# Optimization experiments

Hardware: AMD Instinct MI355X
Metric: run time of the kernel (lower is better)

Reference implementation:

```python
import jax, jax.numpy as jnp
import numpy as np

HID = 1024   # hidden_dim
H = 16       # num_head
D = 64       # head_dim
W = 64       # window_size (one-sided attention radius)


def setup_inputs() -> dict:
    key = jax.random.key(0)
    ks = jax.random.split(key, 10)
    B, S = 2, 4096
    s = 0.02
    X = jax.random.normal(ks[0], (B, S, HID), jnp.float32)
    mask = jnp.ones((B, S), jnp.float32)
    Wq = jax.random.normal(ks[1], (HID, H * D), jnp.float32) * s
    bq = jnp.zeros((H * D,), jnp.float32)
    Wk = jax.random.normal(ks[2], (HID, H * D), jnp.float32) * s
    bk = jnp.zeros((H * D,), jnp.float32)
    Wv = jax.random.normal(ks[3], (HID, H * D), jnp.float32) * s
    bv = jnp.zeros((H * D,), jnp.float32)
    Wo = jax.random.normal(ks[4], (H * D, HID), jnp.float32) * s
    bo = jnp.zeros((HID,), jnp.float32)
    return dict(X=X, mask=mask, Wq=Wq, bq=bq, Wk=Wk, bk=bk, Wv=Wv, bv=bv, Wo=Wo, bo=bo)


def _chunk3(T, nC):
    # T: [B,H,S,D] -> [B,H,nC,3W,D]: for chunk c, keys of chunks c-1, c, c+1 (zero-padded at ends)
    B, Hh, S, Dd = T.shape
    Tp = jnp.pad(T, ((0, 0), (0, 0), (W, W), (0, 0))).reshape(B, Hh, nC + 2, W, Dd)
    return jnp.concatenate([Tp[:, :, :-2], Tp[:, :, 1:-1], Tp[:, :, 2:]], axis=3)


def reference(X, mask, Wq, bq, Wk, bk, Wv, bv, Wo, bo):
    B, S0, _ = X.shape
    pad = W - S0 % W  # matches torch: always >= 1 (full window if divisible)
    Xp = jnp.pad(X, ((0, 0), (0, pad), (0, 0)))
    mp = jnp.pad(mask, ((0, 0), (0, pad)))  # padded keys masked out
    S = S0 + pad
    nC = S // W

    def proj(Wm, b):
        return (Xp @ Wm + b).reshape(B, S, H, D).transpose(0, 2, 1, 3)  # [B,H,S,D]

    Q, K, V = proj(Wq, bq), proj(Wk, bk), proj(Wv, bv)
    Qc = Q.reshape(B, H, nC, W, D)
    K3 = _chunk3(K, nC)
    V3 = _chunk3(V, nC)

    # banded scores: query i attends keys j with |i - j| <= W
    scores = jnp.einsum('bhcqd,bhckd->bhcqk', Qc, K3) / jnp.asarray(np.sqrt(D), jnp.float32)
    qi = jnp.arange(W)[:, None]
    kj = jnp.arange(3 * W)[None, :]
    band = (kj >= qi) & (kj <= qi + 2 * W)  # [W, 3W]
    m3 = jnp.pad(mp, ((0, 0), (W, W))).reshape(B, nC + 2, W)
    m3 = jnp.concatenate([m3[:, :-2], m3[:, 1:-1], m3[:, 2:]], axis=2)  # [B,nC,3W]
    valid = band[None, None, None, :, :] & (m3[:, None, :, None, :] > 0)
    scores = jnp.where(valid, scores, -1e9)
    A = jax.nn.softmax(scores, axis=-1)
    ctx = jnp.einsum('bhcqk,bhckd->bhcqd', A, V3).reshape(B, H, S, D)
    out = ctx.transpose(0, 2, 1, 3).reshape(B, S, H * D) @ Wo + bo
    return out[:, :S0]
```

## Files before the change

kernel.cpp:

```cpp
#include <hip/hip_runtime.h>

typedef unsigned short u16;
typedef unsigned int u32;
typedef __bf16 bf16x8 __attribute__((ext_vector_type(8)));
typedef u16 u16x8 __attribute__((ext_vector_type(8)));
typedef float floatx4 __attribute__((ext_vector_type(4)));

#define MFMA16(a, b, c) __builtin_amdgcn_mfma_f32_16x16x32_bf16((a), (b), (c), 0, 0, 0)

#define B_ 2
#define S0 4096
#define NH 16
#define HD 64
#define HID 1024
#define VSTR 216

__device__ __forceinline__ float bf2f(u16 u) {
  union { u32 i; float f; } x; x.i = ((u32)u) << 16; return x.f;
}
__device__ __forceinline__ u16 f2bf(float f) {
  union { float f; u32 i; } x; x.f = f;
  u32 r = x.i + 0x7FFFu + ((x.i >> 16) & 1u);
  return (u16)(r >> 16);
}

__device__ __forceinline__ void glds16(const u16* g, u16* l) {
  __builtin_amdgcn_global_load_lds(
      (const __attribute__((address_space(1))) u32*)g,
      (__attribute__((address_space(3))) u32*)l, 16, 0, 0);
}

__global__ __launch_bounds__(256) void prep(
    const float* __restrict__ X, const float* __restrict__ mask,
    const float* __restrict__ Wq, const float* __restrict__ bq,
    const float* __restrict__ Wk, const float* __restrict__ bk,
    const float* __restrict__ Wv, const float* __restrict__ bv,
    const float* __restrict__ Wo, const float* __restrict__ bo,
    u16* __restrict__ cX, u16* __restrict__ cmask, u16* __restrict__ cb,
    u16* __restrict__ WqkvT, u16* __restrict__ WoT) {
  __shared__ u16 tile[64][66];
  int bid = blockIdx.x;
  if (bid < 4096) {
    int i = (bid * 256 + threadIdx.x) * 8;
    u16x8 v;
#pragma unroll
    for (int j = 0; j < 8; j++) v[j] = f2bf(X[i + j]);
    *(u16x8*)(cX + i) = v;
  } else if (bid < 4144) {
    int tid = (bid - 4096) * 256 + threadIdx.x;
    if (tid < B_ * S0) {
      cmask[tid] = f2bf(mask[tid]);
    } else {
      int j = tid - B_ * S0;
      int seg = j >> 10, idx = j & 1023;
      const float* src = (seg == 0) ? bq : (seg == 1) ? bk : (seg == 2) ? bv : bo;
      cb[seg * 1024 + idx] = f2bf(src[idx]);
    }
  } else {
    int idx = bid - 4144;
    int mat = idx >> 8;
    const float* src = (mat == 0) ? Wq : (mat == 1) ? Wk : (mat == 2) ? Wv : Wo;
    u16* dst = (mat < 3) ? (WqkvT + (size_t)mat * HID * HID) : WoT;
    int t0 = ((idx >> 4) & 15) * 64;
    int c0 = (idx & 15) * 64;
    int tx = threadIdx.x & 63, ty = threadIdx.x >> 6;
#pragma unroll
    for (int i = 0; i < 16; i++) {
      int r = i * 4 + ty;
      tile[r][tx] = f2bf(src[(size_t)(t0 + r) * HID + c0 + tx]);
    }
    __syncthreads();
#pragma unroll
    for (int i = 0; i < 16; i++) {
      int r = i * 4 + ty;
      dst[(size_t)(c0 + r) * HID + t0 + tx] = tile[tx][r];
    }
  }
}

template <int BN, int MODE>
__global__ __launch_bounds__(256) void gemm_bf16_tn(
    const u16* __restrict__ A, const u16* __restrict__ Bt,
    const u16* __restrict__ cb, void* __restrict__ outp, int K) {
  constexpr int NT = BN / 32;
  __shared__ alignas(16) u16 sA[128 * 64];
  __shared__ alignas(16) u16 sB[BN * 64];
  int t = threadIdx.x;
  int wave = t >> 6, lane = t & 63;
  int wm = wave >> 1, wn = wave & 1;
  int quad = lane >> 4, l16 = lane & 15;
  int tile_m = blockIdx.x * 128;
  int tile_n = blockIdx.y * BN;

  floatx4 acc[4][NT] = {};

  int row_l = lane >> 3;
  int col_l = ((lane & 7) ^ row_l) * 8;
  const u16* Ag = A + (size_t)(tile_m + wave * 8 + row_l) * K + col_l;
  const u16* Bg = Bt + (size_t)(tile_n + wave * 8 + row_l) * K + col_l;
  u16* lA = sA + wave * 8 * 64;
  u16* lB = sB + wave * 8 * 64;

  for (int k0 = 0; k0 < K; k0 += 64) {
    __syncthreads();
#pragma unroll
    for (int r = 0; r < 4; r++)
      glds16(Ag + (size_t)(r * 32) * K + k0, lA + r * 2048);
#pragma unroll
    for (int r = 0; r < BN / 32; r++)
      glds16(Bg + (size_t)(r * 32) * K + k0, lB + r * 2048);
    __syncthreads();

#pragma unroll
    for (int ks = 0; ks < 2; ks++) {
      bf16x8 af[4], bfr[NT];
#pragma unroll
      for (int mt = 0; mt < 4; mt++) {
        int row = wm * 64 + mt * 16 + l16;
        int p = (ks * 4 + quad) ^ (row & 7);
        af[mt] = *(const bf16x8*)(sA + row * 64 + p * 8);
      }
#pragma unroll
      for (int nt = 0; nt < NT; nt++) {
        int row = wn * (BN / 2) + nt * 16 + l16;
        int p = (ks * 4 + quad) ^ (row & 7);
        bfr[nt] = *(const bf16x8*)(sB + row * 64 + p * 8);
      }
#pragma unroll
      for (int mt = 0; mt < 4; mt++)
#pragma unroll
        for (int nt = 0; nt < NT; nt++)
          acc[mt][nt] = MFMA16(af[mt], bfr[nt], acc[mt][nt]);
    }
  }

  if (MODE == 0) {
    u16* op = (u16*)outp;
#pragma unroll
    for (int mt = 0; mt < 4; mt++) {
      int row0 = tile_m + wm * 64 + mt * 16 + quad * 4;
      int bb = row0 >> 12;
      int sbase = row0 & (S0 - 1);
#pragma unroll
      for (int nt = 0; nt < NT; nt++) {
        int col = tile_n + wn * (BN / 2) + nt * 16 + l16;
        int p = col >> 10;
        int rem = col & 1023;
        float bias = bf2f(cb[p * 1024 + rem]);
        int hh = rem >> 6, dd = rem & 63;
        u16* dp = op + ((size_t)(((p * 2 + bb) * NH + hh)) * S0 + sbase) * HD + dd;
#pragma unroll
        for (int r = 0; r < 4; r++)
          dp[(size_t)r * HD] = f2bf(acc[mt][nt][r] + bias);
      }
    }
  } else {
    float* op = (float*)outp;
#pragma unroll
    for (int mt = 0; mt < 4; mt++) {
      int row0 = tile_m + wm * 64 + mt * 16 + quad * 4;
#pragma unroll
      for (int nt = 0; nt < NT; nt++) {
        int col = tile_n + wn * (BN / 2) + nt * 16 + l16;
        float bias = bf2f(cb[3 * 1024 + col]);
        float* dp = op + (size_t)row0 * HID + col;
#pragma unroll
        for (int r = 0; r < 4; r++)
          dp[(size_t)r * HID] = acc[mt][nt][r] + bias;
      }
    }
  }
}

__global__ __launch_bounds__(256) void attn_win(
    const u16* __restrict__ Q, const u16* __restrict__ Kp,
    const u16* __restrict__ Vp, const u16* __restrict__ cmask,
    u16* __restrict__ ctx) {
  __shared__ alignas(16) u16 buf0[64 * VSTR];
  __shared__ alignas(16) u16 sP[4 * 16 * 200];
  __shared__ u16 sMk[208];

  int bid = blockIdx.x;
  int c = bid & 63;
  int h = (bid >> 6) & 15;
  int b = bid >> 10;
  int t = threadIdx.x;
  int wave = t >> 6, lane = t & 63;
  int quad = lane >> 4, l16 = lane & 15;
  int koff = wave * 16;

  const u16* Qb = Q + (size_t)(b * NH + h) * S0 * HD;
  const u16* Kb = Kp + (size_t)(b * NH + h) * S0 * HD;
  const u16* Vb = Vp + (size_t)(b * NH + h) * S0 * HD;
  int kbase = (c - 1) * 64;

  int rrow = lane >> 3;
  int csrc = ((lane & 7) ^ rrow) * 8;
#pragma unroll
  for (int p = 0; p < 7; p++) {
    int sl0 = p * 32 + wave * 8;
    if (sl0 < 208) {
      int key = kbase + sl0 + rrow;
      int kc = key < 0 ? 0 : (key > S0 - 1 ? S0 - 1 : key);
      glds16(Kb + (size_t)kc * HD + csrc, buf0 + sl0 * 64);
    }
  }
  if (t < 208) {
    int j = kbase + t;
    sMk[t] = (j >= 0 && j < S0) ? cmask[(size_t)b * S0 + j] : (u16)0;
  }

  int qrow = c * 64 + wave * 16 + l16;
  bf16x8 aqv[2];
#pragma unroll
  for (int ks = 0; ks < 2; ks++)
    aqv[ks] = *(const bf16x8*)(Qb + (size_t)qrow * HD + ks * 32 + quad * 8);

  __syncthreads();

  floatx4 sc[9] = {};
  __builtin_amdgcn_s_setprio(1);
#pragma unroll
  for (int ks = 0; ks < 2; ks++) {
#pragma unroll
    for (int nt = 0; nt < 9; nt++) {
      int slot = koff + nt * 16 + l16;
      int pch = ((ks * 4 + quad) ^ (l16 & 7)) * 8;
      bf16x8 bk = *(const bf16x8*)(buf0 + slot * 64 + pch);
      sc[nt] = MFMA16(aqv[ks], bk, sc[nt]);
    }
  }
  __builtin_amdgcn_s_setprio(0);

  u16x8 vreg[7];
#pragma unroll
  for (int i = 0; i < 7; i++) {
    int e = i * 256 + t;
    if (e < 1664) {
      int dg = e / 208;
      int slot = e - dg * 208;
      int key = kbase + slot;
      int kc = key < 0 ? 0 : (key > S0 - 1 ? S0 - 1 : key);
      vreg[i] = *(const u16x8*)(Vb + (size_t)kc * HD + dg * 8);
    }
  }

  int qrel_base = wave * 16 + quad * 4;
  u16* myP = sP + wave * 16 * 200;
  float kmask[9];
#pragma unroll
  for (int nt = 0; nt < 9; nt++) kmask[nt] = bf2f(sMk[koff + nt * 16 + l16]);

#pragma unroll
  for (int reg = 0; reg < 4; reg++) {
    int qrel = qrel_base + reg;
    float v[9];
    float m = -3e38f;
#pragma unroll
    for (int nt = 0; nt < 9; nt++) {
      int slot = koff + nt * 16 + l16;
      bool ok = (slot >= qrel) && (slot <= qrel + 128) && (kmask[nt] > 0.f);
      float s = ok ? sc[nt][reg] * 0.125f : -1e30f;
      v[nt] = s;
      m = fmaxf(m, s);
    }
#pragma unroll
    for (int off = 1; off <= 8; off <<= 1) m = fmaxf(m, __shfl_xor(m, off));
    float sum = 0.f;
#pragma unroll
    for (int nt = 0; nt < 9; nt++) {
      float p = __expf(v[nt] - m);
      v[nt] = p;
      sum += p;
    }
#pragma unroll
    for (int off = 1; off <= 8; off <<= 1) sum += __shfl_xor(sum, off);
    float inv = 1.0f / sum;
    int prow = (quad * 4 + reg) * 200;
#pragma unroll
    for (int nt = 0; nt < 9; nt++)
      myP[prow + nt * 16 + l16] = f2bf(v[nt] * inv);
    myP[prow + 144 + l16] = 0;
  }
  __syncthreads();

#pragma unroll
  for (int i = 0; i < 7; i++) {
    int e = i * 256 + t;
    if (e < 1664) {
      int dg = e / 208;
      int slot = e - dg * 208;
#pragma unroll
      for (int j = 0; j < 8; j++) buf0[(dg * 8 + j) * VSTR + slot] = vreg[i][j];
    }
  }
  __syncthreads();

  floatx4 oc[4] = {};
  __builtin_amdgcn_s_setprio(1);
#pragma unroll
  for (int ks = 0; ks < 5; ks++) {
    bf16x8 ap = *(const bf16x8*)(myP + l16 * 200 + ks * 32 + quad * 8);
#pragma unroll
    for (int nt = 0; nt < 4; nt++) {
      bf16x8 bv =
          *(const bf16x8*)(buf0 + (nt * 16 + l16) * VSTR + koff + ks * 32 + quad * 8);
      oc[nt] = MFMA16(ap, bv, oc[nt]);
    }
  }
  __builtin_amdgcn_s_setprio(0);

  int srow = c * 64 + wave * 16 + quad * 4;
#pragma unroll
  for (int nt = 0; nt < 4; nt++) {
    u16* dp = ctx + (size_t)(b * S0 + srow) * HID + h * HD + nt * 16 + l16;
#pragma unroll
    for (int reg = 0; reg < 4; reg++)
      dp[(size_t)reg * HID] = f2bf(oc[nt][reg]);
  }
}

extern "C" void kernel_launch(void* const* d_in, const int* in_sizes, int n_in,
                              void* d_out, int out_size, void* d_ws, size_t ws_size,
                              hipStream_t stream) {
  const float* X = (const float*)d_in[0];
  const float* mask = (const float*)d_in[1];
  const float* Wq = (const float*)d_in[2];
  const float* bq = (const float*)d_in[3];
  const float* Wk = (const float*)d_in[4];
  const float* bk = (const float*)d_in[5];
  const float* Wv = (const float*)d_in[6];
  const float* bv = (const float*)d_in[7];
  const float* Wo = (const float*)d_in[8];
  const float* bo = (const float*)d_in[9];
  char* ws = (char*)d_ws;

  const size_t MB = 1048576;
  u16* cmask = (u16*)(ws + 256);
  u16* cb = (u16*)(ws + 256 + 16384);
  u16* cX = (u16*)(ws + 1 * MB);
  u16* WqkvT = (u16*)(ws + 17 * MB);
  u16* WoT = (u16*)(ws + 23 * MB);
  u16* QKV = (u16*)(ws + 25 * MB);
  u16* CTX = cX;

  const size_t per_qkv = (size_t)B_ * NH * S0 * HD;

  prep<<<4096 + 48 + 1024, 256, 0, stream>>>(X, mask, Wq, bq, Wk, bk, Wv, bv,
                                             Wo, bo, cX, cmask, cb, WqkvT, WoT);
  gemm_bf16_tn<128, 0><<<dim3(64, 24), 256, 0, stream>>>(cX, WqkvT, cb, QKV, HID);
  attn_win<<<dim3(B_ * NH * 64), 256, 0, stream>>>(QKV, QKV + per_qkv,
                                                   QKV + 2 * per_qkv, cmask, CTX);
  gemm_bf16_tn<128, 1><<<dim3(64, 8), 256, 0, stream>>>(CTX, WoT, cb, d_out, HID);
}
```

Measured before the change: 229.7 us.

## Replace QKV GEMM with 256x256 tile eight-phase double-buffered pipelined kernel

Adds a dedicated QKV projection GEMM that uses 512-thread blocks and 256x256 output tiles. It double-buffers LDS and interleaves global-to-LDS loads with MFMA phases, using explicit barriers and vmcnt waits to overlap memory and compute. The old templated GEMM is specialized to the output projection only. The attention P-buffer stride also shrinks from 200 to 184, which changes the LDS bank pattern and footprint. The larger tiles give more reuse per tile but only 384 blocks, and the fine-grained barrier schedule is fragile.

```diff
diff --git a/kernel.cpp b/kernel.cpp
--- a/kernel.cpp
+++ b/kernel.cpp
@@ -14,6 +14,7 @@
 #define HD 64
 #define HID 1024
 #define VSTR 216
+#define PSTR 184
 
 __device__ __forceinline__ float bf2f(u16 u) {
   union { u32 i; float f; } x; x.i = ((u32)u) << 16; return x.f;
@@ -78,10 +79,153 @@
   }
 }
 
-template <int BN, int MODE>
+#define NTILE 16
+
+#define STAGE_A(kt, half)                                                  \
+  do {                                                                     \
+    if ((kt) < NTILE) {                                                    \
+      _Pragma("unroll") for (int i_ = 0; i_ < 2; i_++) {                   \
+        int r0_ = (half) * 64 + i_ * 128 + wave * 8;                       \
+        glds16(Ag + (size_t)r0_ * 1024 + (kt) * 64,                        \
+               &sA[(kt) & 1][r0_ * 64]);                                   \
+      }                                                                    \
+    }                                                                      \
+  } while (0)
+
+#define STAGE_B(kt, odd)                                                   \
+  do {                                                                     \
+    if ((kt) < NTILE) {                                                    \
+      _Pragma("unroll") for (int i_ = 0; i_ < 2; i_++) {                   \
+        int g_ = wave * 16 + i_ * 8;                                       \
+        int r0_ = (g_ >> 5) * 64 + (odd) * 32 + (g_ & 31);                 \
+        glds16(Bg + (size_t)r0_ * 1024 + (kt) * 64,                        \
+               &sB[(kt) & 1][r0_ * 64]);                                   \
+      }                                                                    \
+    }                                                                      \
+  } while (0)
+
+#define READ_A(mh)                                                         \
+  do {                                                                     \
+    _Pragma("unroll") for (int mi_ = 0; mi_ < 4; mi_++) {                  \
+      int row_ = wm * 128 + (mh) * 64 + mi_ * 16 + l16;                    \
+      af[mi_][0] = *(const bf16x8*)(&sA[bi][row_ * 64 + xk0]);             \
+      af[mi_][1] = *(const bf16x8*)(&sA[bi][row_ * 64 + xk1]);             \
+    }                                                                      \
+  } while (0)
+
+#define READ_B(arr, nh)                                                    \
+  do {                                                                     \
+    _Pragma("unroll") for (int ni_ = 0; ni_ < 2; ni_++) {                  \
+      int row_ = wn * 64 + (nh) * 32 + ni_ * 16 + l16;                     \
+      arr[ni_][0] = *(const bf16x8*)(&sB[bi][row_ * 64 + xk0]);            \
+      arr[ni_][1] = *(const bf16x8*)(&sB[bi][row_ * 64 + xk1]);            \
+    }                                                                      \
+  } while (0)
+
+#define PHASE_BAR1()                                                       \
+  __builtin_amdgcn_sched_barrier(0);                                       \
+  __builtin_amdgcn_s_barrier();                                            \
+  asm volatile("s_waitcnt lgkmcnt(0)" ::: "memory");                       \
+  __builtin_amdgcn_sched_barrier(0)
+
+#define MFMA_PH(mh, nh, barr)                                              \
+  do {                                                                     \
+    __builtin_amdgcn_s_setprio(1);                                         \
+    _Pragma("unroll") for (int ks_ = 0; ks_ < 2; ks_++)                    \
+        _Pragma("unroll") for (int mi_ = 0; mi_ < 4; mi_++)                \
+            _Pragma("unroll") for (int ni_ = 0; ni_ < 2; ni_++)            \
+                acc[(mh) * 4 + mi_][(nh) * 2 + ni_] =                      \
+        MFMA16(af[mi_][ks_], barr[ni_][ks_],                               \
+               acc[(mh) * 4 + mi_][(nh) * 2 + ni_]);                       \
+    __builtin_amdgcn_s_setprio(0);                                         \
+    __builtin_amdgcn_sched_barrier(0);                                     \
+    __builtin_amdgcn_s_barrier();                                          \
+    __builtin_amdgcn_sched_barrier(0);                                     \
+  } while (0)
+
+__global__ __launch_bounds__(512, 2) void gemm_qkv_8ph(
+    const u16* __restrict__ A, const u16* __restrict__ Bt,
+    const u16* __restrict__ cb, u16* __restrict__ op) {
+  __shared__ alignas(16) u16 sA[2][256 * 64];
+  __shared__ alignas(16) u16 sB[2][256 * 64];
+  int t = threadIdx.x;
+  int wave = t >> 6, lane = t & 63;
+  int quad = lane >> 4, l16 = lane & 15;
+  int wm = wave >> 2, wn = wave & 3;
+  int tile_m = blockIdx.x * 256;
+  int tile_n = blockIdx.y * 256;
+
+  floatx4 acc[8][4] = {};
+  bf16x8 af[4][2], bn0[2][2], bn1[2][2];
+
+  int srow = lane >> 3;
+  int scol = ((lane & 7) ^ srow) * 8;
+  const u16* Ag = A + (size_t)(tile_m + srow) * 1024 + scol;
+  const u16* Bg = Bt + (size_t)(tile_n + srow) * 1024 + scol;
+
+  int xk0 = (quad ^ (l16 & 7)) * 8;
+  int xk1 = ((4 + quad) ^ (l16 & 7)) * 8;
+
+  STAGE_A(0, 0);
+  STAGE_B(0, 0);
+  STAGE_B(0, 1);
+  STAGE_A(0, 1);
+  STAGE_A(1, 0);
+  STAGE_B(1, 0);
+  STAGE_B(1, 1);
+  asm volatile("s_waitcnt vmcnt(6)" ::: "memory");
+  __builtin_amdgcn_s_barrier();
+  __builtin_amdgcn_sched_barrier(0);
+
+  for (int T = 0; T < NTILE; ++T) {
+    int bi = T & 1;
+    READ_A(0);
+    READ_B(bn0, 0);
+    STAGE_A(T + 1, 1);
+    PHASE_BAR1();
+    MFMA_PH(0, 0, bn0);
+    READ_B(bn1, 1);
+    STAGE_A(T + 2, 0);
+    PHASE_BAR1();
+    MFMA_PH(0, 1, bn1);
+    READ_A(1);
+    STAGE_B(T + 2, 0);
+    PHASE_BAR1();
+    MFMA_PH(1, 1, bn1);
+    STAGE_B(T + 2, 1);
+    if (T < NTILE - 2) {
+      asm volatile("s_waitcnt vmcnt(6)" ::: "memory");
+    } else {
+      asm volatile("s_waitcnt vmcnt(0)" ::: "memory");
+    }
+    PHASE_BAR1();
+    MFMA_PH(1, 0, bn0);
+  }
+
+#pragma unroll
+  for (int mf = 0; mf < 8; mf++) {
+    int row0 = tile_m + wm * 128 + mf * 16 + quad * 4;
+    int bb = row0 >> 12;
+    int sbase = row0 & (S0 - 1);
+#pragma unroll
+    for (int nf = 0; nf < 4; nf++) {
+      int col = tile_n + wn * 64 + nf * 16 + l16;
+      int p = col >> 10;
+      int rem = col & 1023;
+      float bias = bf2f(cb[p * 1024 + rem]);
+      int hh = rem >> 6, dd = rem & 63;
+      u16* dp = op + ((size_t)(((p * 2 + bb) * NH + hh)) * S0 + sbase) * HD + dd;
+#pragma unroll
+      for (int r = 0; r < 4; r++)
+        dp[(size_t)r * HD] = f2bf(acc[mf][nf][r] + bias);
+    }
+  }
+}
+
 __global__ __launch_bounds__(256) void gemm_bf16_tn(
     const u16* __restrict__ A, const u16* __restrict__ Bt,
-    const u16* __restrict__ cb, void* __restrict__ outp, int K) {
+    const u16* __restrict__ cb, float* __restrict__ op, int K) {
+  constexpr int BN = 128;
   constexpr int NT = BN / 32;
   __shared__ alignas(16) u16 sA[128 * 64];
   __shared__ alignas(16) u16 sB[BN * 64];
@@ -134,40 +278,17 @@
     }
   }
 
-  if (MODE == 0) {
-    u16* op = (u16*)outp;
-#pragma unroll
-    for (int mt = 0; mt < 4; mt++) {
-      int row0 = tile_m + wm * 64 + mt * 16 + quad * 4;
-      int bb = row0 >> 12;
-      int sbase = row0 & (S0 - 1);
-#pragma unroll
-      for (int nt = 0; nt < NT; nt++) {
-        int col = tile_n + wn * (BN / 2) + nt * 16 + l16;
-        int p = col >> 10;
-        int rem = col & 1023;
-        float bias = bf2f(cb[p * 1024 + rem]);
-        int hh = rem >> 6, dd = rem & 63;
-        u16* dp = op + ((size_t)(((p * 2 + bb) * NH + hh)) * S0 + sbase) * HD + dd;
-#pragma unroll
-        for (int r = 0; r < 4; r++)
-          dp[(size_t)r * HD] = f2bf(acc[mt][nt][r] + bias);
-      }
-    }
-  } else {
-    float* op = (float*)outp;
-#pragma unroll
-    for (int mt = 0; mt < 4; mt++) {
-      int row0 = tile_m + wm * 64 + mt * 16 + quad * 4;
-#pragma unroll
-      for (int nt = 0; nt < NT; nt++) {
-        int col = tile_n + wn * (BN / 2) + nt * 16 + l16;
-        float bias = bf2f(cb[3 * 1024 + col]);
-        float* dp = op + (size_t)row0 * HID + col;
-#pragma unroll
-        for (int r = 0; r < 4; r++)
-          dp[(size_t)r * HID] = acc[mt][nt][r] + bias;
-      }
+#pragma unroll
+  for (int mt = 0; mt < 4; mt++) {
+    int row0 = tile_m + wm * 64 + mt * 16 + quad * 4;
+#pragma unroll
+    for (int nt = 0; nt < NT; nt++) {
+      int col = tile_n + wn * (BN / 2) + nt * 16 + l16;
+      float bias = bf2f(cb[3 * 1024 + col]);
+      float* dp = op + (size_t)row0 * HID + col;
+#pragma unroll
+      for (int r = 0; r < 4; r++)
+        dp[(size_t)r * HID] = acc[mt][nt][r] + bias;
     }
   }
 }
@@ -177,7 +298,7 @@
     const u16* __restrict__ Vp, const u16* __restrict__ cmask,
     u16* __restrict__ ctx) {
   __shared__ alignas(16) u16 buf0[64 * VSTR];
-  __shared__ alignas(16) u16 sP[4 * 16 * 200];
+  __shared__ alignas(16) u16 sP[4 * 16 * PSTR];
   __shared__ u16 sMk[208];
 
   int bid = blockIdx.x;
@@ -246,7 +367,7 @@
   }
 
   int qrel_base = wave * 16 + quad * 4;
-  u16* myP = sP + wave * 16 * 200;
+  u16* myP = sP + wave * 16 * PSTR;
   float kmask[9];
 #pragma unroll
   for (int nt = 0; nt < 9; nt++) kmask[nt] = bf2f(sMk[koff + nt * 16 + l16]);
@@ -276,7 +397,7 @@
 #pragma unroll
     for (int off = 1; off <= 8; off <<= 1) sum += __shfl_xor(sum, off);
     float inv = 1.0f / sum;
-    int prow = (quad * 4 + reg) * 200;
+    int prow = (quad * 4 + reg) * PSTR;
 #pragma unroll
     for (int nt = 0; nt < 9; nt++)
       myP[prow + nt * 16 + l16] = f2bf(v[nt] * inv);
@@ -300,7 +421,7 @@
   __builtin_amdgcn_s_setprio(1);
 #pragma unroll
   for (int ks = 0; ks < 5; ks++) {
-    bf16x8 ap = *(const bf16x8*)(myP + l16 * 200 + ks * 32 + quad * 8);
+    bf16x8 ap = *(const bf16x8*)(myP + l16 * PSTR + ks * 32 + quad * 8);
 #pragma unroll
     for (int nt = 0; nt < 4; nt++) {
       bf16x8 bv =
@@ -348,8 +469,8 @@
 
   prep<<<4096 + 48 + 1024, 256, 0, stream>>>(X, mask, Wq, bq, Wk, bk, Wv, bv,
                                              Wo, bo, cX, cmask, cb, WqkvT, WoT);
-  gemm_bf16_tn<128, 0><<<dim3(64, 24), 256, 0, stream>>>(cX, WqkvT, cb, QKV, HID);
+  gemm_qkv_8ph<<<dim3(32, 12), 512, 0, stream>>>(cX, WqkvT, cb, QKV);
   attn_win<<<dim3(B_ * NH * 64), 256, 0, stream>>>(QKV, QKV + per_qkv,
                                                    QKV + 2 * per_qkv, cmask, CTX);
-  gemm_bf16_tn<128, 1><<<dim3(64, 8), 256, 0, stream>>>(CTX, WoT, cb, d_out, HID);
-}
+  gemm_bf16_tn<<<dim3(64, 8), 256, 0, stream>>>(CTX, WoT, cb, (float*)d_out, HID);
+}
```

New measurement: 234.2 us. No clear change (+2.0%).
